# Kernel optimization log

Measured on AMD Instinct MI355X. Metric: run time of the kernel, lower is better.

The kernel has to match this reference:

```python
import jax, jax.numpy as jnp
from jax import lax
import numpy as np

K_LIST = [2, 4, 8]

def setup_inputs() -> dict:
    key = jax.random.key(0)
    k1, k2 = jax.random.split(key)
    B_, C, H, Wd = 8, 256, 128, 128
    x = jax.random.normal(k1, (B_, C, H, Wd), dtype=jnp.float32)
    # conv weights init ~ N(0, 1e-6) per the module's 'zero' init, bias zero
    W = jax.random.normal(k2, (len(K_LIST), 1, C, 3, 3), dtype=jnp.float32) * 1e-6
    Bb = jnp.zeros((len(K_LIST), 1), dtype=jnp.float32)
    return {"x": x, "W": W, "B": Bb}


def _band_grid(h, w):
    # signed max of (fftfreq_h, rfftfreq_w) coords, matching torch code
    fh = jnp.fft.fftfreq(h).astype(jnp.float32)          # [h]
    fw = jnp.fft.rfftfreq(w).astype(jnp.float32)         # [w//2+1]
    return jnp.maximum(fh[:, None], fw[None, :])         # [h, w//2+1]


def reference(x, W, B):
    b, c, h, w = x.shape
    x_dtype = x.dtype
    x32 = x.astype(jnp.float32)
    x_fft = jnp.fft.rfft2(x32, norm='ortho')             # [b,c,h,w//2+1] complex
    grid = _band_grid(h, w)
    pre_x = x32
    out = jnp.zeros_like(x32)
    for idx, freq in enumerate(K_LIST):
        mask = (grid < 0.5 / freq).astype(jnp.float32)   # [h, w//2+1]
        low = jnp.fft.irfft2(x_fft * mask, s=(h, w), norm='ortho')
        high = pre_x - low
        pre_x = low
        # Conv2d(in=256, out=1, k=3, pad=1) on att_feat=x
        fwgt = lax.conv_general_dilated(
            x32, W[idx], window_strides=(1, 1), padding='SAME',
            dimension_numbers=('NCHW', 'OIHW', 'NCHW'))
        fwgt = fwgt + B[idx][None, :, None, None]        # [b,1,h,w]
        gate = jax.nn.sigmoid(fwgt) * 2.0
        out = out + gate * high                          # broadcast over channels
    out = out + pre_x                                    # residual low-frequency part
    return out.astype(x_dtype)
```

## Files before the change

kernel.cpp:

```cpp
#include <hip/hip_runtime.h>


#define NPIX 16384
#define NCHN 256

typedef __attribute__((ext_vector_type(8))) short bf16x8;
typedef __attribute__((ext_vector_type(4))) float f32x4;

__device__ __align__(16) short g_f[64][128];
__device__ __align__(16) short g_h[192][256];
__device__ __align__(16) short g_e[3][256][192];
__device__ __align__(16) short g_p[3][128][64];

static __device__ __forceinline__ short f2bf(float f) {
  unsigned u = __float_as_uint(f);
  unsigned r = (u + 0x7fffu + ((u >> 16) & 1u)) >> 16;
  return (short)r;
}
static __device__ __forceinline__ float bf2f(short s) {
  return __uint_as_float(((unsigned)(unsigned short)s) << 16);
}
static __device__ __forceinline__ f32x4 mfma16(bf16x8 a, bf16x8 b, f32x4 c) {
  return __builtin_amdgcn_mfma_f32_16x16x32_bf16(a, b, c, 0, 0, 0);
}

__global__ __launch_bounds__(256) void const_init_kernel() {
  int idx = blockIdx.x * 256 + threadIdx.x;
  const float C = 6.2831853071795864769f / 128.f;
  if (idx < 8192) {
    int n = idx >> 7, q = idx & 127;
    int j = n & 31;
    float ang = C * (float)((j * q) & 127);
    float v = (n < 32) ? cosf(ang) : -sinf(ang);
    reinterpret_cast<short*>(g_f)[idx] = f2bf(v);
  } else if (idx < 57344) {
    int e = idx - 8192;
    int d = e >> 8, kk = e & 255;
    int r = (d < 96) ? d : d - 96;
    int ifr = (r < 32) ? r : r + 32;
    float ang = C * (float)((ifr * (kk & 127)) & 127);
    float cv = cosf(ang) * (1.f / 128.f), sv = sinf(ang) * (1.f / 128.f);
    float v = (d < 96) ? ((kk < 128) ? cv : sv) : ((kk < 128) ? -sv : cv);
    reinterpret_cast<short*>(g_h)[e] = f2bf(v);
  } else if (idx < 204800) {
    int e = idx - 57344;
    int k = e / 49152; int e2 = e % 49152;
    int mm = e2 / 192, kk = e2 % 192;
    int nk = 32 >> k;
    int r = (kk < 96) ? kk : kk - 96;
    bool allow = (r < nk) || (r >= 32);
    int ifr = (r < 32) ? r : r + 32;
    float ang = C * (float)((ifr * (mm & 127)) & 127);
    float cv = cosf(ang), sv = sinf(ang);
    float v = (mm < 128) ? ((kk < 96) ? cv : -sv) : ((kk < 96) ? sv : cv);
    reinterpret_cast<short*>(g_e)[e] = f2bf(allow ? v : 0.f);
  } else {
    int e = idx - 204800;
    int k = e / 8192; int e2 = e % 8192;
    int n = e2 >> 6, jj = e2 & 63;
    int nk = 32 >> k;
    int j = jj & 31;
    bool valid = (j < nk) && (jj < 32 || j > 0);
    float wj = (j == 0) ? (1.f / 128.f) : (2.f / 128.f);
    float ang = C * (float)((j * n) & 127);
    float v = (jj < 32) ? (wj * cosf(ang)) : (-wj * sinf(ang));
    reinterpret_cast<short*>(g_p)[e] = f2bf(valid ? v : 0.f);
  }
}

__global__ __launch_bounds__(256) void gates_partial_kernel(
    const float* __restrict__ x, const float* __restrict__ Wg,
    float* __restrict__ partial) {
  int bid = blockIdx.x;
  int b = bid & 7;
  int tile = (bid >> 3) & 63;
  int cs = bid >> 9;
  int m = ((tile >> 3) << 4) + (threadIdx.x >> 4);
  int n = ((tile & 7) << 4) + (threadIdx.x & 15);
  float a0 = 0.f, a1 = 0.f, a2 = 0.f;
  const float* xb = x + (size_t)b * NCHN * NPIX;
  for (int c = cs * 64; c < cs * 64 + 64; ++c) {
    const float* xc = xb + (size_t)c * NPIX;
    const float* wc = Wg + c * 9;
    #pragma unroll
    for (int dh = -1; dh <= 1; ++dh) {
      int gm = m + dh;
      bool vm = (unsigned)gm < 128u;
      #pragma unroll
      for (int dw = -1; dw <= 1; ++dw) {
        int gn = n + dw;
        float xv = (vm && (unsigned)gn < 128u) ? xc[gm * 128 + gn] : 0.f;
        int tap = (dh + 1) * 3 + (dw + 1);
        a0 = fmaf(xv, wc[tap], a0);
        a1 = fmaf(xv, wc[2304 + tap], a1);
        a2 = fmaf(xv, wc[4608 + tap], a2);
      }
    }
  }
  int pix = m * 128 + n;
  float* pp = partial + (size_t)(cs * 8 + b) * 3 * NPIX;
  pp[pix]            = a0;
  pp[NPIX + pix]     = a1;
  pp[2 * NPIX + pix] = a2;
}

__global__ __launch_bounds__(256) void gates_combine_kernel(
    const float* __restrict__ partial, const float* __restrict__ Bg,
    short* __restrict__ dcoef) {
  int bid = blockIdx.x;
  int b = bid & 7;
  int px = (bid >> 3) * 256 + threadIdx.x;
  float a0 = Bg[0], a1 = Bg[1], a2 = Bg[2];
  #pragma unroll
  for (int cs = 0; cs < 4; ++cs) {
    const float* pp = partial + (size_t)(cs * 8 + b) * 3 * NPIX;
    a0 += pp[px];
    a1 += pp[NPIX + px];
    a2 += pp[2 * NPIX + px];
  }
  float g1 = 2.f / (1.f + expf(-a0));
  float g2 = 2.f / (1.f + expf(-a1));
  float g3 = 2.f / (1.f + expf(-a2));
  int pix = b * NPIX + px;
  dcoef[pix]          = f2bf(g1 - 1.f);
  dcoef[131072 + pix] = f2bf(g2 - g1);
  dcoef[262144 + pix] = f2bf(g3 - g2);
  dcoef[393216 + pix] = f2bf(1.f - g3);
}

__global__ __launch_bounds__(256) void gates_kernel(
    const float* __restrict__ x, const float* __restrict__ Wg,
    const float* __restrict__ Bg, short* __restrict__ dcoef) {
  int blk = blockIdx.x;
  int b = blk >> 6;
  int tile = blk & 63;
  int m = ((tile >> 3) << 4) + (threadIdx.x >> 4);
  int n = ((tile & 7) << 4) + (threadIdx.x & 15);
  float a0 = 0.f, a1 = 0.f, a2 = 0.f;
  const float* xb = x + (size_t)b * NCHN * NPIX;
  for (int c = 0; c < NCHN; ++c) {
    const float* xc = xb + (size_t)c * NPIX;
    const float* wc = Wg + c * 9;
    #pragma unroll
    for (int dh = -1; dh <= 1; ++dh) {
      int gm = m + dh;
      bool vm = (unsigned)gm < 128u;
      #pragma unroll
      for (int dw = -1; dw <= 1; ++dw) {
        int gn = n + dw;
        float xv = (vm && (unsigned)gn < 128u) ? xc[gm * 128 + gn] : 0.f;
        int tap = (dh + 1) * 3 + (dw + 1);
        a0 = fmaf(xv, wc[tap], a0);
        a1 = fmaf(xv, wc[2304 + tap], a1);
        a2 = fmaf(xv, wc[4608 + tap], a2);
      }
    }
  }
  a0 += Bg[0]; a1 += Bg[1]; a2 += Bg[2];
  float g1 = 2.f / (1.f + expf(-a0));
  float g2 = 2.f / (1.f + expf(-a1));
  float g3 = 2.f / (1.f + expf(-a2));
  int pix = b * NPIX + m * 128 + n;
  dcoef[pix]          = f2bf(g1 - 1.f);
  dcoef[131072 + pix] = f2bf(g2 - g1);
  dcoef[262144 + pix] = f2bf(g3 - g2);
  dcoef[393216 + pix] = f2bf(1.f - g3);
}

__global__ __launch_bounds__(512, 2) void fbm_kernel(
    const float* __restrict__ x, const short* __restrict__ dcoef,
    float* __restrict__ out) {
  __shared__ __align__(16) short Xs[16384];
  __shared__ __align__(16) short WVs[8192];
  __shared__ __align__(16) short Ds2[6144];
  char* XsB = reinterpret_cast<char*>(Xs);
  char* PlaneB = XsB;
  char* WsB = reinterpret_cast<char*>(WVs);
  char* DsB = reinterpret_cast<char*>(Ds2);

  int t = threadIdx.x;
  int bid = blockIdx.x;
  int b = bid >> 6;
  int cg = bid & 63;
  size_t img0 = ((size_t)b << 8) + ((size_t)cg << 2);
  int lane = t & 63, w = t >> 6;
  int l15 = lane & 15, l4 = lane >> 4;
  const f32x4 zero = {0.f, 0.f, 0.f, 0.f};

  const short4* d0p = reinterpret_cast<const short4*>(dcoef + ((size_t)b << 14));

  for (int c = 0; c < 4; ++c) {
    f32x4 oaccC[8];
    {
      const f32x4* xv4 = reinterpret_cast<const f32x4*>(x + (img0 + c) * NPIX);
      #pragma unroll
      for (int i = 0; i < 8; ++i) {
        int f = t + i * 512;
        f32x4 xv = __builtin_nontemporal_load(&xv4[f]);
        short4 dv = d0p[f];
        f32x4 dvf = {bf2f(dv.x), bf2f(dv.y), bf2f(dv.z), bf2f(dv.w)};
        oaccC[i] = xv + dvf * xv;
        int row = f >> 5;
        int byte = row * 256 + (((f & 31) * 8) ^ ((row & 7) << 4));
        short4 s;
        s.x = f2bf(xv[0]); s.y = f2bf(xv[1]); s.z = f2bf(xv[2]); s.w = f2bf(xv[3]);
        *reinterpret_cast<short4*>(XsB + byte) = s;
      }
    }
    __syncthreads();

    {
      int Ntile = w & 3, Mq = w >> 2;
      int n = Ntile * 16 + l15;
      f32x4 acc[4] = {zero, zero, zero, zero};
      #pragma unroll
      for (int ks = 0; ks < 4; ++ks) {
        int koff = ks * 32 + l4 * 8;
        bf16x8 bf = *reinterpret_cast<const bf16x8*>(&g_f[n][koff]);
        #pragma unroll
        for (int mt = 0; mt < 4; ++mt) {
          int p = (Mq * 4 + mt) * 16 + l15;
          bf16x8 a = *reinterpret_cast<const bf16x8*>(
              XsB + p * 256 + ((koff * 2) ^ ((p & 7) << 4)));
          acc[mt] = mfma16(a, bf, acc[mt]);
        }
      }
      #pragma unroll
      for (int mt = 0; mt < 4; ++mt) {
        int p0 = (Mq * 4 + mt) * 16 + l4 * 4;
        short4 s;
        s.x = f2bf(acc[mt][0]); s.y = f2bf(acc[mt][1]);
        s.z = f2bf(acc[mt][2]); s.w = f2bf(acc[mt][3]);
        *reinterpret_cast<short4*>(WsB + n * 256 + ((p0 * 2) ^ ((n & 7) << 4))) = s;
      }
    }
    __syncthreads();

    {
      int Ntile = w & 1, Mt3 = w >> 1;
      int n = Ntile * 16 + l15;
      f32x4 acc[3] = {zero, zero, zero};
      #pragma unroll
      for (int ks = 0; ks < 8; ++ks) {
        int koff = ks * 32 + l4 * 8;
        int wrow = n + ((ks >= 4) ? 32 : 0);
        bf16x8 bb = *reinterpret_cast<const bf16x8*>(
            WsB + wrow * 256 + (((koff & 127) * 2) ^ ((wrow & 7) << 4)));
        #pragma unroll
        for (int mt = 0; mt < 3; ++mt) {
          int d = (Mt3 * 3 + mt) * 16 + l15;
          bf16x8 aa = *reinterpret_cast<const bf16x8*>(&g_h[d][koff]);
          acc[mt] = mfma16(aa, bb, acc[mt]);
        }
      }
      #pragma unroll
      for (int mt = 0; mt < 3; ++mt) {
        int d0 = (Mt3 * 3 + mt) * 16 + l4 * 4;
        short4 s;
        s.x = f2bf(acc[mt][0]); s.y = f2bf(acc[mt][1]);
        s.z = f2bf(acc[mt][2]); s.w = f2bf(acc[mt][3]);
        *reinterpret_cast<short4*>(DsB + n * 384 + ((d0 * 2) ^ ((n & 7) << 4))) = s;
      }
    }
    __syncthreads();

    int Mg3 = w >> 2, Ng3 = w & 3;
    for (int k = 0; k < 3; ++k) {
      {
        f32x4 acc[2][2] = {{zero, zero}, {zero, zero}};
        #pragma unroll
        for (int ks = 0; ks < 6; ++ks) {
          int koff = ks * 32 + l4 * 8;
          bf16x8 b0 = *reinterpret_cast<const bf16x8*>(
              DsB + l15 * 384 + ((koff * 2) ^ ((l15 & 7) << 4)));
          int j1 = 16 + l15;
          bf16x8 b1 = *reinterpret_cast<const bf16x8*>(
              DsB + j1 * 384 + ((koff * 2) ^ ((j1 & 7) << 4)));
          #pragma unroll
          for (int mi = 0; mi < 2; ++mi) {
            int mstk = (2 * w + mi) * 16 + l15;
            bf16x8 aa = *reinterpret_cast<const bf16x8*>(&g_e[k][mstk][koff]);
            acc[mi][0] = mfma16(aa, b0, acc[mi][0]);
            acc[mi][1] = mfma16(aa, b1, acc[mi][1]);
          }
        }
        #pragma unroll
        for (int mi = 0; mi < 2; ++mi) {
          #pragma unroll
          for (int ni = 0; ni < 2; ++ni) {
            int j = ni * 16 + l15;
            #pragma unroll
            for (int r = 0; r < 4; ++r) {
              int mstk = (2 * w + mi) * 16 + l4 * 4 + r;
              int m = mstk & 127;
              int jst = ((mstk >> 7) << 5) + j;
              *reinterpret_cast<short*>(WsB + m * 128 + ((jst * 2) ^ ((m & 7) << 4))) =
                  f2bf(acc[mi][ni][r]);
            }
          }
        }
      }
      __syncthreads();
      {
        f32x4 acc[4][2] = {{zero, zero}, {zero, zero}, {zero, zero}, {zero, zero}};
        #pragma unroll
        for (int ks = 0; ks < 2; ++ks) {
          int koff = ks * 32 + l4 * 8;
          bf16x8 bfr[2];
          #pragma unroll
          for (int nt = 0; nt < 2; ++nt) {
            int nout = (Ng3 * 2 + nt) * 16 + l15;
            bfr[nt] = *reinterpret_cast<const bf16x8*>(&g_p[k][nout][koff]);
          }
          #pragma unroll
          for (int mt = 0; mt < 4; ++mt) {
            int m = (Mg3 * 4 + mt) * 16 + l15;
            bf16x8 aa = *reinterpret_cast<const bf16x8*>(
                WsB + m * 128 + ((koff * 2) ^ ((m & 7) << 4)));
            acc[mt][0] = mfma16(aa, bfr[0], acc[mt][0]);
            acc[mt][1] = mfma16(aa, bfr[1], acc[mt][1]);
          }
        }
        #pragma unroll
        for (int mt = 0; mt < 4; ++mt) {
          #pragma unroll
          for (int nt = 0; nt < 2; ++nt) {
            int col = (Ng3 * 2 + nt) * 16 + l15;
            #pragma unroll
            for (int r = 0; r < 4; ++r) {
              int row = (Mg3 * 4 + mt) * 16 + l4 * 4 + r;
              int byte = row * 256 + ((col ^ ((row & 7) << 2)) << 1);
              *reinterpret_cast<short*>(PlaneB + byte) = f2bf(acc[mt][nt][r]);
            }
          }
        }
      }
      __syncthreads();
      {
        const short4* dk = reinterpret_cast<const short4*>(
            dcoef + (size_t)(k + 1) * 131072 + ((size_t)b << 14));
        #pragma unroll
        for (int i = 0; i < 8; ++i) {
          int f = t + i * 512;
          int row = f >> 5;
          int col = (f & 31) * 4;
          int byte = row * 256 + ((col ^ ((row & 7) << 2)) << 1);
          short4 s = *reinterpret_cast<const short4*>(PlaneB + byte);
          short4 dv = dk[f];
          oaccC[i][0] = fmaf(bf2f(dv.x), bf2f(s.x), oaccC[i][0]);
          oaccC[i][1] = fmaf(bf2f(dv.y), bf2f(s.y), oaccC[i][1]);
          oaccC[i][2] = fmaf(bf2f(dv.z), bf2f(s.z), oaccC[i][2]);
          oaccC[i][3] = fmaf(bf2f(dv.w), bf2f(s.w), oaccC[i][3]);
        }
      }
      __syncthreads();
    }

    f32x4* og4 = reinterpret_cast<f32x4*>(out + (img0 + c) * NPIX);
    #pragma unroll
    for (int i = 0; i < 8; ++i) og4[t + i * 512] = oaccC[i];
  }
}

extern "C" void kernel_launch(void* const* d_in, const int* in_sizes, int n_in,
                              void* d_out, int out_size, void* d_ws, size_t ws_size,
                              hipStream_t stream) {
  const float* x  = (const float*)d_in[0];
  const float* Wg = (const float*)d_in[1];
  const float* Bg = (const float*)d_in[2];
  float* out  = (float*)d_out;
  short* dcoef = (short*)d_ws;
  float* partial = (float*)((char*)d_ws + (1u << 20));
  const_init_kernel<<<896, 256, 0, stream>>>();
  if (ws_size >= (size_t)(8u << 20)) {
    gates_partial_kernel<<<2048, 256, 0, stream>>>(x, Wg, partial);
    gates_combine_kernel<<<512, 256, 0, stream>>>(partial, Bg, dcoef);
  } else {
    gates_kernel<<<512, 256, 0, stream>>>(x, Wg, Bg, dcoef);
  }
  fbm_kernel<<<512, 512, 0, stream>>>(x, dcoef, out);
}
```

Measured before the change: 309.7 us.

## Batch the three band stages into separate LDS buffers to cut barriers

Each block now gives every band k its own LDS buffer for the intermediate V matrix and the reconstructed plane. The three stage-A GEMMs, then the three stage-B GEMMs, then one combined gated accumulation each run under a single barrier, instead of syncing after every sub-step for each band. This removes about six __syncthreads per channel and lets independent MFMA work interleave. The cost is shared memory rising from about 60 KB to about 156 KB per block, which likely allows only one 512-thread block per CU instead of the two the launch bounds target.

```diff
diff --git a/kernel.cpp b/kernel.cpp
--- a/kernel.cpp
+++ b/kernel.cpp
@@ -170,13 +170,14 @@
 __global__ __launch_bounds__(512, 2) void fbm_kernel(
     const float* __restrict__ x, const short* __restrict__ dcoef,
     float* __restrict__ out) {
-  __shared__ __align__(16) short Xs[16384];
-  __shared__ __align__(16) short WVs[8192];
-  __shared__ __align__(16) short Ds2[6144];
-  char* XsB = reinterpret_cast<char*>(Xs);
-  char* PlaneB = XsB;
-  char* WsB = reinterpret_cast<char*>(WVs);
-  char* DsB = reinterpret_cast<char*>(Ds2);
+  __shared__ __align__(16) short SH[79872];
+  char* AB = reinterpret_cast<char*>(SH);
+  char* BB = reinterpret_cast<char*>(SH + 16384);
+  char* CB = reinterpret_cast<char*>(SH + 24576);
+  char* DB = reinterpret_cast<char*>(SH + 30720);
+  char* EB = reinterpret_cast<char*>(SH + 47104);
+  char* VBp[3] = {BB, DB, DB + 16384};
+  char* PLp[3] = {EB, AB, EB + 32768};
 
   int t = threadIdx.x;
   int bid = blockIdx.x;
@@ -204,7 +205,7 @@
         int byte = row * 256 + (((f & 31) * 8) ^ ((row & 7) << 4));
         short4 s;
         s.x = f2bf(xv[0]); s.y = f2bf(xv[1]); s.z = f2bf(xv[2]); s.w = f2bf(xv[3]);
-        *reinterpret_cast<short4*>(XsB + byte) = s;
+        *reinterpret_cast<short4*>(AB + byte) = s;
       }
     }
     __syncthreads();
@@ -221,7 +222,7 @@
         for (int mt = 0; mt < 4; ++mt) {
           int p = (Mq * 4 + mt) * 16 + l15;
           bf16x8 a = *reinterpret_cast<const bf16x8*>(
-              XsB + p * 256 + ((koff * 2) ^ ((p & 7) << 4)));
+              AB + p * 256 + ((koff * 2) ^ ((p & 7) << 4)));
           acc[mt] = mfma16(a, bf, acc[mt]);
         }
       }
@@ -231,7 +232,7 @@
         short4 s;
         s.x = f2bf(acc[mt][0]); s.y = f2bf(acc[mt][1]);
         s.z = f2bf(acc[mt][2]); s.w = f2bf(acc[mt][3]);
-        *reinterpret_cast<short4*>(WsB + n * 256 + ((p0 * 2) ^ ((n & 7) << 4))) = s;
+        *reinterpret_cast<short4*>(BB + n * 256 + ((p0 * 2) ^ ((n & 7) << 4))) = s;
       }
     }
     __syncthreads();
@@ -245,7 +246,7 @@
         int koff = ks * 32 + l4 * 8;
         int wrow = n + ((ks >= 4) ? 32 : 0);
         bf16x8 bb = *reinterpret_cast<const bf16x8*>(
-            WsB + wrow * 256 + (((koff & 127) * 2) ^ ((wrow & 7) << 4)));
+            BB + wrow * 256 + (((koff & 127) * 2) ^ ((wrow & 7) << 4)));
         #pragma unroll
         for (int mt = 0; mt < 3; ++mt) {
           int d = (Mt3 * 3 + mt) * 16 + l15;
@@ -259,49 +260,55 @@
         short4 s;
         s.x = f2bf(acc[mt][0]); s.y = f2bf(acc[mt][1]);
         s.z = f2bf(acc[mt][2]); s.w = f2bf(acc[mt][3]);
-        *reinterpret_cast<short4*>(DsB + n * 384 + ((d0 * 2) ^ ((n & 7) << 4))) = s;
-      }
-    }
-    __syncthreads();
-
-    int Mg3 = w >> 2, Ng3 = w & 3;
+        *reinterpret_cast<short4*>(CB + n * 384 + ((d0 * 2) ^ ((n & 7) << 4))) = s;
+      }
+    }
+    __syncthreads();
+
+    #pragma unroll
     for (int k = 0; k < 3; ++k) {
-      {
-        f32x4 acc[2][2] = {{zero, zero}, {zero, zero}};
-        #pragma unroll
-        for (int ks = 0; ks < 6; ++ks) {
-          int koff = ks * 32 + l4 * 8;
-          bf16x8 b0 = *reinterpret_cast<const bf16x8*>(
-              DsB + l15 * 384 + ((koff * 2) ^ ((l15 & 7) << 4)));
-          int j1 = 16 + l15;
-          bf16x8 b1 = *reinterpret_cast<const bf16x8*>(
-              DsB + j1 * 384 + ((koff * 2) ^ ((j1 & 7) << 4)));
+      char* VB = VBp[k];
+      f32x4 acc[2][2] = {{zero, zero}, {zero, zero}};
+      #pragma unroll
+      for (int ks = 0; ks < 6; ++ks) {
+        int koff = ks * 32 + l4 * 8;
+        bf16x8 b0 = *reinterpret_cast<const bf16x8*>(
+            CB + l15 * 384 + ((koff * 2) ^ ((l15 & 7) << 4)));
+        int j1 = 16 + l15;
+        bf16x8 b1 = *reinterpret_cast<const bf16x8*>(
+            CB + j1 * 384 + ((koff * 2) ^ ((j1 & 7) << 4)));
+        #pragma unroll
+        for (int mi = 0; mi < 2; ++mi) {
+          int mstk = (2 * w + mi) * 16 + l15;
+          bf16x8 aa = *reinterpret_cast<const bf16x8*>(&g_e[k][mstk][koff]);
+          acc[mi][0] = mfma16(aa, b0, acc[mi][0]);
+          acc[mi][1] = mfma16(aa, b1, acc[mi][1]);
+        }
+      }
+      #pragma unroll
+      for (int mi = 0; mi < 2; ++mi) {
+        #pragma unroll
+        for (int ni = 0; ni < 2; ++ni) {
+          int j = ni * 16 + l15;
           #pragma unroll
-          for (int mi = 0; mi < 2; ++mi) {
-            int mstk = (2 * w + mi) * 16 + l15;
-            bf16x8 aa = *reinterpret_cast<const bf16x8*>(&g_e[k][mstk][koff]);
-            acc[mi][0] = mfma16(aa, b0, acc[mi][0]);
-            acc[mi][1] = mfma16(aa, b1, acc[mi][1]);
+          for (int r = 0; r < 4; ++r) {
+            int mstk = (2 * w + mi) * 16 + l4 * 4 + r;
+            int m = mstk & 127;
+            int jst = ((mstk >> 7) << 5) + j;
+            *reinterpret_cast<short*>(VB + m * 128 + ((jst * 2) ^ ((m & 7) << 4))) =
+                f2bf(acc[mi][ni][r]);
           }
         }
-        #pragma unroll
-        for (int mi = 0; mi < 2; ++mi) {
-          #pragma unroll
-          for (int ni = 0; ni < 2; ++ni) {
-            int j = ni * 16 + l15;
-            #pragma unroll
-            for (int r = 0; r < 4; ++r) {
-              int mstk = (2 * w + mi) * 16 + l4 * 4 + r;
-              int m = mstk & 127;
-              int jst = ((mstk >> 7) << 5) + j;
-              *reinterpret_cast<short*>(WsB + m * 128 + ((jst * 2) ^ ((m & 7) << 4))) =
-                  f2bf(acc[mi][ni][r]);
-            }
-          }
-        }
-      }
-      __syncthreads();
-      {
+      }
+    }
+    __syncthreads();
+
+    {
+      int Mg3 = w >> 2, Ng3 = w & 3;
+      #pragma unroll
+      for (int k = 0; k < 3; ++k) {
+        char* VB = VBp[k];
+        char* PL = PLp[k];
         f32x4 acc[4][2] = {{zero, zero}, {zero, zero}, {zero, zero}, {zero, zero}};
         #pragma unroll
         for (int ks = 0; ks < 2; ++ks) {
@@ -316,7 +323,7 @@
           for (int mt = 0; mt < 4; ++mt) {
             int m = (Mg3 * 4 + mt) * 16 + l15;
             bf16x8 aa = *reinterpret_cast<const bf16x8*>(
-                WsB + m * 128 + ((koff * 2) ^ ((m & 7) << 4)));
+                VB + m * 128 + ((koff * 2) ^ ((m & 7) << 4)));
             acc[mt][0] = mfma16(aa, bfr[0], acc[mt][0]);
             acc[mt][1] = mfma16(aa, bfr[1], acc[mt][1]);
           }
@@ -330,31 +337,48 @@
             for (int r = 0; r < 4; ++r) {
               int row = (Mg3 * 4 + mt) * 16 + l4 * 4 + r;
               int byte = row * 256 + ((col ^ ((row & 7) << 2)) << 1);
-              *reinterpret_cast<short*>(PlaneB + byte) = f2bf(acc[mt][nt][r]);
+              *reinterpret_cast<short*>(PL + byte) = f2bf(acc[mt][nt][r]);
             }
           }
         }
       }
-      __syncthreads();
-      {
-        const short4* dk = reinterpret_cast<const short4*>(
-            dcoef + (size_t)(k + 1) * 131072 + ((size_t)b << 14));
-        #pragma unroll
-        for (int i = 0; i < 8; ++i) {
-          int f = t + i * 512;
-          int row = f >> 5;
-          int col = (f & 31) * 4;
-          int byte = row * 256 + ((col ^ ((row & 7) << 2)) << 1);
-          short4 s = *reinterpret_cast<const short4*>(PlaneB + byte);
-          short4 dv = dk[f];
-          oaccC[i][0] = fmaf(bf2f(dv.x), bf2f(s.x), oaccC[i][0]);
-          oaccC[i][1] = fmaf(bf2f(dv.y), bf2f(s.y), oaccC[i][1]);
-          oaccC[i][2] = fmaf(bf2f(dv.z), bf2f(s.z), oaccC[i][2]);
-          oaccC[i][3] = fmaf(bf2f(dv.w), bf2f(s.w), oaccC[i][3]);
-        }
-      }
-      __syncthreads();
-    }
+    }
+    __syncthreads();
+
+    {
+      const short4* dk1 = reinterpret_cast<const short4*>(
+          dcoef + (size_t)131072 + ((size_t)b << 14));
+      const short4* dk2 = reinterpret_cast<const short4*>(
+          dcoef + (size_t)262144 + ((size_t)b << 14));
+      const short4* dk3 = reinterpret_cast<const short4*>(
+          dcoef + (size_t)393216 + ((size_t)b << 14));
+      #pragma unroll
+      for (int i = 0; i < 8; ++i) {
+        int f = t + i * 512;
+        int row = f >> 5;
+        int col = (f & 31) * 4;
+        int byte = row * 256 + ((col ^ ((row & 7) << 2)) << 1);
+        short4 s0 = *reinterpret_cast<const short4*>(PLp[0] + byte);
+        short4 s1 = *reinterpret_cast<const short4*>(PLp[1] + byte);
+        short4 s2 = *reinterpret_cast<const short4*>(PLp[2] + byte);
+        short4 dv1 = dk1[f];
+        short4 dv2 = dk2[f];
+        short4 dv3 = dk3[f];
+        oaccC[i][0] = fmaf(bf2f(dv1.x), bf2f(s0.x), oaccC[i][0]);
+        oaccC[i][1] = fmaf(bf2f(dv1.y), bf2f(s0.y), oaccC[i][1]);
+        oaccC[i][2] = fmaf(bf2f(dv1.z), bf2f(s0.z), oaccC[i][2]);
+        oaccC[i][3] = fmaf(bf2f(dv1.w), bf2f(s0.w), oaccC[i][3]);
+        oaccC[i][0] = fmaf(bf2f(dv2.x), bf2f(s1.x), oaccC[i][0]);
+        oaccC[i][1] = fmaf(bf2f(dv2.y), bf2f(s1.y), oaccC[i][1]);
+        oaccC[i][2] = fmaf(bf2f(dv2.z), bf2f(s1.z), oaccC[i][2]);
+        oaccC[i][3] = fmaf(bf2f(dv2.w), bf2f(s1.w), oaccC[i][3]);
+        oaccC[i][0] = fmaf(bf2f(dv3.x), bf2f(s2.x), oaccC[i][0]);
+        oaccC[i][1] = fmaf(bf2f(dv3.y), bf2f(s2.y), oaccC[i][1]);
+        oaccC[i][2] = fmaf(bf2f(dv3.z), bf2f(s2.z), oaccC[i][2]);
+        oaccC[i][3] = fmaf(bf2f(dv3.w), bf2f(s2.w), oaccC[i][3]);
+      }
+    }
+    __syncthreads();
 
     f32x4* og4 = reinterpret_cast<f32x4*>(out + (img0 + c) * NPIX);
     #pragma unroll
```

New measurement: 465.3 us. +50.3%, slower.
